# Kernel optimization log

Hardware: AMD Instinct MI355X
Metric: run time of the kernel (lower is better)

## Reference

```python
import jax, jax.numpy as jnp
import numpy as np

N, C, H, W = 512, 512, 7, 7
K = 64
ALPHA = 100.0
HW = H * W


def _up13(x):
    # bilinear upsample (..., 7, 7) -> (..., 13, 13), align_corners=True
    src = jnp.arange(13, dtype=jnp.float32) * (6.0 / 12.0)
    i0 = jnp.floor(src).astype(jnp.int32)
    i1 = jnp.minimum(i0 + 1, 6)
    w = src - i0.astype(jnp.float32)
    xr = x[..., i0, :] * (1.0 - w)[:, None] + x[..., i1, :] * w[:, None]  # rows
    xc = xr[..., :, i0] * (1.0 - w) + xr[..., :, i1] * w                  # cols
    return xc


def _conv2d(x, w, b, p):
    y = jax.lax.conv_general_dilated(
        x, w, window_strides=(1, 1), padding=[(p, p), (p, p)],
        dimension_numbers=('NCHW', 'OIHW', 'NCHW'))
    return y + b[None, :, None, None]


def setup_inputs() -> dict:
    key = jax.random.key(0)
    ks = jax.random.split(key, 16)
    x = jax.random.normal(ks[0], (N, C, H, W), jnp.float32)
    centroids = jax.random.uniform(ks[1], (K, C), jnp.float32)
    # conv params initialized from centroids as in _init_params (separate params after init)
    conv_w = 2.0 * ALPHA * centroids                    # (K, C) 1x1 conv kernel
    conv_b = -ALPHA * jnp.linalg.norm(centroids, axis=1)
    ln_w = jnp.ones((7, 7), jnp.float32)
    ln_b = jnp.zeros((7, 7), jnp.float32)
    c3_w = 0.02 * jax.random.normal(ks[2], (32, 512, 3, 3), jnp.float32)
    c3_b = jnp.zeros((32,), jnp.float32)
    c5_w = 0.02 * jax.random.normal(ks[3], (32, 512, 5, 5), jnp.float32)
    c5_b = jnp.zeros((32,), jnp.float32)
    c7_w = 0.02 * jax.random.normal(ks[4], (20, 512, 7, 7), jnp.float32)
    c7_b = jnp.zeros((20,), jnp.float32)
    dw_w = 0.1 * jax.random.normal(ks[5], (7, 13), jnp.float32)
    dw_b = jnp.zeros((7,), jnp.float32)
    dh_w = 0.1 * jax.random.normal(ks[6], (7, 13), jnp.float32)
    dh_b = jnp.zeros((7,), jnp.float32)
    acc_w = 0.1 * jax.random.normal(ks[7], (1, 84), jnp.float32)  # 1x1 conv (O, I)
    acc_b = jnp.zeros((1,), jnp.float32)
    return dict(x=x, centroids=centroids, conv_w=conv_w, conv_b=conv_b,
                ln_w=ln_w, ln_b=ln_b, c3_w=c3_w, c3_b=c3_b, c5_w=c5_w, c5_b=c5_b,
                c7_w=c7_w, c7_b=c7_b, dw_w=dw_w, dw_b=dw_b, dh_w=dh_w, dh_b=dh_b,
                acc_w=acc_w, acc_b=acc_b)


def reference(x, centroids, conv_w, conv_b, ln_w, ln_b,
              c3_w, c3_b, c5_w, c5_b, c7_w, c7_b,
              dw_w, dw_b, dh_w, dh_b, acc_w, acc_b):
    # ---- CRN on the raw (un-normalized) input ----
    mu = jnp.mean(x, axis=(-2, -1), keepdims=True)
    var = jnp.mean((x - mu) ** 2, axis=(-2, -1), keepdims=True)
    h = (x - mu) / jnp.sqrt(var + 1e-5) * ln_w + ln_b          # LayerNorm([7,7])
    h = _up13(h)                                               # (N,512,13,13)
    h = jnp.concatenate([_conv2d(h, c3_w, c3_b, 1),
                         _conv2d(h, c5_w, c5_b, 2),
                         _conv2d(h, c7_w, c7_b, 3)], axis=1)   # (N,84,13,13)
    h = jnp.einsum('nchw,ow->ncho', h, dw_w) + dw_b            # width 13->7
    h = h.transpose(0, 1, 3, 2)
    h = jnp.einsum('nchw,ow->ncho', h, dh_w) + dh_b            # height 13->7
    cw = jnp.einsum('nchw,oc->nohw', h, acc_w) + acc_b[None, :, None, None]
    cw = cw.reshape(N, 1, HW)                                  # context weights

    # ---- descriptor-wise L2 normalization over channels ----
    nrm = jnp.sqrt(jnp.sum(x * x, axis=1, keepdims=True))
    xn = x / jnp.maximum(nrm, 1e-12)

    # ---- soft assignment (1x1 conv + softmax over clusters) ----
    logits = (jnp.einsum('nchw,kc->nkhw', xn, conv_w)
              + conv_b[None, :, None, None]).reshape(N, K, HW)
    sa = jax.nn.softmax(logits, axis=1)
    mask = sa * cw                                             # (N,K,HW)

    # ---- fused VLAD aggregation (same math as masked residual sum) ----
    xf = xn.reshape(N, C, HW)
    vlad = jnp.einsum('nkl,ncl->nkc', mask, xf) \
        - centroids[None, :, :] * jnp.sum(mask, axis=-1)[:, :, None]
    vlad = vlad / jnp.maximum(jnp.linalg.norm(vlad, axis=2, keepdims=True), 1e-12)
    vlad = vlad.reshape(N, K * C)
    vlad = vlad / jnp.maximum(jnp.linalg.norm(vlad, axis=1, keepdims=True), 1e-12)
    return vlad
```

## Files before the change

kernel.cpp:

```cpp
#include <hip/hip_runtime.h>
#include <math.h>

#define NI 512
#define CC 512
#define KCL 64
#define HW49 49
#define CQ 25088
#define XHP 260
#define AP 260
#define GP 68
#define NKS 256

__device__ __forceinline__ float Uval(int i, int u) {
    if (i & 1) return (u == ((i - 1) >> 1) || u == ((i + 1) >> 1)) ? 0.5f : 0.0f;
    return (u == (i >> 1)) ? 1.0f : 0.0f;
}

__global__ __launch_bounds__(256) void kG(
    const float* __restrict__ c3w, const float* __restrict__ c5w, const float* __restrict__ c7w,
    const float* __restrict__ dww, const float* __restrict__ dhw, const float* __restrict__ accw,
    const float* __restrict__ lnw, const float* __restrict__ lnb,
    float* __restrict__ Gmat, float* __restrict__ Gl)
{
    const int c = blockIdx.x;
    const int t = threadIdx.x;
    __shared__ float dh[91], dw[91];
    __shared__ float Fh3[147], Fw3[147], Fh5[245], Fw5[245], Fh7[343], Fw7[343];
    __shared__ float wa3[9], wa5[25], wa7[49];
    __shared__ float Gtmp[2401];
    if (t < 91) dh[t] = dhw[t];
    if (t >= 128 && t < 219) dw[t - 128] = dww[t - 128];
    __syncthreads();
    for (int idx = t; idx < 147; idx += 256) {
        int oh = idx / 21, r = idx % 21, u = r / 3, dy = r % 3;
        float sh = 0.f, sw = 0.f;
        for (int i = 0; i < 13; i++) { int y = i - dy + 1; if (y >= 0 && y < 13) { float uu = Uval(i, u); sh += dh[oh * 13 + y] * uu; sw += dw[oh * 13 + y] * uu; } }
        Fh3[idx] = sh; Fw3[idx] = sw;
    }
    for (int idx = t; idx < 245; idx += 256) {
        int oh = idx / 35, r = idx % 35, u = r / 5, dy = r % 5;
        float sh = 0.f, sw = 0.f;
        for (int i = 0; i < 13; i++) { int y = i - dy + 2; if (y >= 0 && y < 13) { float uu = Uval(i, u); sh += dh[oh * 13 + y] * uu; sw += dw[oh * 13 + y] * uu; } }
        Fh5[idx] = sh; Fw5[idx] = sw;
    }
    for (int idx = t; idx < 343; idx += 256) {
        int oh = idx / 49, r = idx % 49, u = r / 7, dy = r % 7;
        float sh = 0.f, sw = 0.f;
        for (int i = 0; i < 13; i++) { int y = i - dy + 3; if (y >= 0 && y < 13) { float uu = Uval(i, u); sh += dh[oh * 13 + y] * uu; sw += dw[oh * 13 + y] * uu; } }
        Fh7[idx] = sh; Fw7[idx] = sw;
    }
    if (t < 9)               { float s = 0.f; for (int co = 0; co < 32; co++) s += accw[co]      * c3w[(size_t)(co * 512 + c) * 9  + t];        wa3[t] = s; }
    if (t >= 32 && t < 57)   { int q = t - 32; float s = 0.f; for (int co = 0; co < 32; co++) s += accw[32 + co] * c5w[(size_t)(co * 512 + c) * 25 + q]; wa5[q] = s; }
    if (t >= 64 && t < 113)  { int q = t - 64; float s = 0.f; for (int co = 0; co < 20; co++) s += accw[64 + co] * c7w[(size_t)(co * 512 + c) * 49 + q]; wa7[q] = s; }
    __syncthreads();
    for (int o = t; o < 2401; o += 256) {
        int q = o / 49, p = o % 49;
        int u = q / 7, v = q % 7, ow = p / 7, oh = p % 7;
        float acc = 0.f;
        #pragma unroll
        for (int dy = 0; dy < 3; dy++) { float fh = Fh3[(oh * 7 + u) * 3 + dy];
            #pragma unroll
            for (int dx = 0; dx < 3; dx++) acc += wa3[dy * 3 + dx] * fh * Fw3[(ow * 7 + v) * 3 + dx]; }
        #pragma unroll
        for (int dy = 0; dy < 5; dy++) { float fh = Fh5[(oh * 7 + u) * 5 + dy];
            #pragma unroll
            for (int dx = 0; dx < 5; dx++) acc += wa5[dy * 5 + dx] * fh * Fw5[(ow * 7 + v) * 5 + dx]; }
        #pragma unroll
        for (int dy = 0; dy < 7; dy++) { float fh = Fh7[(oh * 7 + u) * 7 + dy];
            #pragma unroll
            for (int dx = 0; dx < 7; dx++) acc += wa7[dy * 7 + dx] * fh * Fw7[(ow * 7 + v) * 7 + dx]; }
        Gtmp[o] = acc;
        Gmat[(size_t)c * 2401 + o] = acc * lnw[q];
    }
    __syncthreads();
    if (t < 49) {
        float s = 0.f;
        for (int q = 0; q < 49; q++) s += Gtmp[q * 49 + t] * lnb[q];
        Gl[c * 49 + t] = s;
    }
}

__global__ void kCb(const float* __restrict__ c3b, const float* __restrict__ c5b, const float* __restrict__ c7b,
                    const float* __restrict__ dww, const float* __restrict__ dwb,
                    const float* __restrict__ dhw, const float* __restrict__ dhb,
                    const float* __restrict__ accw, const float* __restrict__ accb,
                    const float* __restrict__ Gl, float* __restrict__ Cb)
{
    __shared__ float A0s, A1s, Sdw[7], Sdh[7];
    int t = threadIdx.x;
    if (t == 0) {
        float a0 = 0.f, a1 = 0.f;
        for (int co = 0; co < 84; co++) {
            float aw = accw[co]; a0 += aw;
            float b = (co < 32) ? c3b[co] : ((co < 64) ? c5b[co - 32] : c7b[co - 64]);
            a1 += aw * b;
        }
        A0s = a0; A1s = a1;
    }
    if (t < 7)             { float s = 0.f; for (int xx = 0; xx < 13; xx++) s += dww[t * 13 + xx]; Sdw[t] = s; }
    if (t >= 8 && t < 15)  { int oh = t - 8; float s = 0.f; for (int y = 0; y < 13; y++) s += dhw[oh * 13 + y]; Sdh[oh] = s; }
    __syncthreads();
    if (t < 49) {
        int ow = t / 7, oh = t % 7;
        float g = 0.f;
        for (int c = 0; c < 512; c++) g += Gl[c * 49 + t];
        Cb[t] = A1s * Sdw[ow] * Sdh[oh] + A0s * (dwb[ow] * Sdh[oh] + dhb[oh]) + accb[0] + g;
    }
}

__global__ __launch_bounds__(256) void kCw1(const float* __restrict__ x,
    const float* __restrict__ Gmat, float* __restrict__ part)
{
    __shared__ float As[49 * AP];
    __shared__ float Gs[49 * GP];
    const int b = blockIdx.x;
    const int nt = b >> 8, ks = b & 255;
    const int n0 = nt * 256;
    const int t = threadIdx.x;
    const int tn = t >> 3;
    const int tp = t & 7;
    float acc[8][8];
    #pragma unroll
    for (int j = 0; j < 8; j++)
        #pragma unroll
        for (int m = 0; m < 8; m++) acc[j][m] = 0.f;
    for (int kk = 0; kk < 2; kk++) {
        const int c = ks * 2 + kk;
        for (int i = t; i < 12544; i += 256) {
            int nr = i / 49, q = i - nr * 49;
            As[q * AP + nr] = x[(size_t)(n0 + nr) * CQ + (size_t)c * 49 + q];
        }
        for (int i = t; i < 2401; i += 256) {
            int q = i / 49, p = i - q * 49;
            Gs[q * GP + p] = Gmat[(size_t)c * 2401 + i];
        }
        for (int i = t; i < 735; i += 256) {
            int q = i / 15, pc = 49 + (i - q * 15);
            Gs[q * GP + pc] = 0.f;
        }
        __syncthreads();
        {
            float s = 0.f, ss = 0.f;
            for (int q = 0; q < 49; q++) { float v = As[q * AP + t]; s += v; ss += v * v; }
            float mu = s * (1.f / 49.f);
            float var = ss * (1.f / 49.f) - mu * mu;
            float rs = 1.f / sqrtf(var + 1e-5f);
            for (int q = 0; q < 49; q++) As[q * AP + t] = (As[q * AP + t] - mu) * rs;
        }
        __syncthreads();
        for (int q = 0; q < 49; q++) {
            float4 a0 = *(const float4*)&As[q * AP + tn * 8];
            float4 a1 = *(const float4*)&As[q * AP + tn * 8 + 4];
            float4 g0 = *(const float4*)&Gs[q * GP + tp * 8];
            float4 g1 = *(const float4*)&Gs[q * GP + tp * 8 + 4];
            float av[8] = {a0.x, a0.y, a0.z, a0.w, a1.x, a1.y, a1.z, a1.w};
            float gv[8] = {g0.x, g0.y, g0.z, g0.w, g1.x, g1.y, g1.z, g1.w};
            #pragma unroll
            for (int j = 0; j < 8; j++)
                #pragma unroll
                for (int m = 0; m < 8; m++) acc[j][m] += av[j] * gv[m];
        }
        __syncthreads();
    }
    #pragma unroll
    for (int j = 0; j < 8; j++) {
        #pragma unroll
        for (int m = 0; m < 8; m++) {
            int p = tp * 8 + m;
            if (p < 49) As[(tn * 8 + j) * 49 + p] = acc[j][m];
        }
    }
    __syncthreads();
    {
        float* dst = part + (size_t)ks * CQ + (size_t)n0 * 49;
        for (int i = t; i < 12544; i += 256) dst[i] = As[i];
    }
}

__global__ __launch_bounds__(512, 2) void kMain(const float* __restrict__ x,
    const float* __restrict__ convw, const float* __restrict__ convb,
    const float* __restrict__ part, const float* __restrict__ Cbg,
    const float* __restrict__ cent, float* __restrict__ out)
{
    __shared__ float xH[49 * XHP];
    __shared__ float lg[64 * 52];
    __shared__ float ps[8 * 56];
    __shared__ float rn[49], cwl[49], smax[49], sinv[49];
    __shared__ float cb[64];
    __shared__ float pmx[392], psm[392];
    __shared__ float msL[64], ssq[64], scl[64];
    const int n = blockIdx.x;
    const int t = threadIdx.x;
    const int lane = t & 63;
    const int w = t >> 6;
    const float* xp = x + (size_t)n * CQ;

    if (t < 392) {
        int p = t >> 3, q = t & 7;
        const float* bp = part + (size_t)n * 49 + p;
        float s = 0.f;
        for (int ks = q * 32; ks < q * 32 + 32; ks++) s += bp[(size_t)ks * CQ];
        psm[t] = s;
    }
    if (t >= 448) cb[t - 448] = convb[t - 448];
    __syncthreads();
    if (t < 49) {
        float s = Cbg[t];
        #pragma unroll
        for (int q = 0; q < 8; q++) s += psm[t * 8 + q];
        cwl[t] = s;
    }

    float a[8];
    #pragma unroll
    for (int j = 0; j < 8; j++) a[j] = 0.f;
    float rs_part = 0.f;
    const int kw = __builtin_amdgcn_readfirstlane(w);

    for (int half = 0; half < 2; half++) {
        const int cbase = half * 256;
        __syncthreads();
        for (int idx = t; idx < 3136; idx += 512) {
            int l = idx % 49, cg = idx / 49;
            const float* src = xp + (size_t)(cbase + cg * 4) * 49 + l;
            float4 v;
            v.x = src[0]; v.y = src[49]; v.z = src[98]; v.w = src[147];
            *(float4*)&xH[l * XHP + cg * 4] = v;
        }
        __syncthreads();
        if (lane < 49) {
            const float* row = &xH[lane * XHP + kw * 32];
            float s = 0.f;
            #pragma unroll
            for (int c4 = 0; c4 < 8; c4++) {
                float4 v = *(const float4*)(row + c4 * 4);
                s += v.x * v.x + v.y * v.y + v.z * v.z + v.w * v.w;
            }
            rs_part += s;
        }
        {
            const int lr = (lane < 49) ? lane : 48;
            const float* xrow = &xH[lr * XHP];
            const float* wb = convw + (size_t)(kw * 8) * 512 + cbase;
            #pragma unroll 4
            for (int c4 = 0; c4 < 64; c4++) {
                float4 xv = *(const float4*)(xrow + c4 * 4);
                #pragma unroll
                for (int j = 0; j < 8; j++) {
                    float4 wv = *(const float4*)&wb[(size_t)j * 512 + c4 * 4];
                    a[j] += wv.x * xv.x + wv.y * xv.y + wv.z * xv.z + wv.w * xv.w;
                }
            }
        }
    }
    if (lane < 49) ps[kw * 56 + lane] = rs_part;
    __syncthreads();
    if (t < 49) {
        float s = 0.f;
        #pragma unroll
        for (int q = 0; q < 8; q++) s += ps[q * 56 + t];
        rn[t] = 1.f / fmaxf(sqrtf(s), 1e-12f);
    }
    __syncthreads();
    if (lane < 49) {
        float r = rn[lane];
        #pragma unroll
        for (int j = 0; j < 8; j++) lg[(kw * 8 + j) * 52 + lane] = a[j] * r + cb[kw * 8 + j];
    }
    __syncthreads();
    if (t < 392) {
        int l = t >> 3, kq = t & 7;
        float m = -3.402823466e38f;
        #pragma unroll
        for (int j = 0; j < 8; j++) m = fmaxf(m, lg[(kq * 8 + j) * 52 + l]);
        pmx[t] = m;
    }
    __syncthreads();
    if (t < 49) {
        float m = pmx[t * 8];
        #pragma unroll
        for (int q = 1; q < 8; q++) m = fmaxf(m, pmx[t * 8 + q]);
        smax[t] = m;
    }
    __syncthreads();
    if (t < 392) {
        int l = t >> 3, kq = t & 7;
        float m = smax[l], s = 0.f;
        #pragma unroll
        for (int j = 0; j < 8; j++) s += __expf(lg[(kq * 8 + j) * 52 + l] - m);
        psm[t] = s;
    }
    __syncthreads();
    if (t < 49) {
        float s = 0.f;
        #pragma unroll
        for (int q = 0; q < 8; q++) s += psm[t * 8 + q];
        sinv[t] = 1.f / s;
    }
    __syncthreads();
    if (t < 392) {
        int l = t >> 3, kq = t & 7;
        float m = smax[l], si = sinv[l] * cwl[l];
        #pragma unroll
        for (int j = 0; j < 8; j++) {
            int idx = (kq * 8 + j) * 52 + l;
            lg[idx] = __expf(lg[idx] - m) * si;
        }
    }
    __syncthreads();
    if (t < 64) {
        float s = 0.f;
        for (int l = 0; l < 49; l++) s += lg[t * 52 + l];
        msL[t] = s;
    }
    __syncthreads();
    if (t < 392) {
        int l = t >> 3, kq = t & 7;
        float r = rn[l];
        #pragma unroll
        for (int j = 0; j < 8; j++) lg[(kq * 8 + j) * 52 + l] *= r;
    }
    __syncthreads();
    const int c0 = lane * 4;
    float accB[8][4], accA[8][4];
    #pragma unroll
    for (int j = 0; j < 8; j++)
        #pragma unroll
        for (int ci = 0; ci < 4; ci++) { accB[j][ci] = 0.f; accA[j][ci] = 0.f; }
    #pragma unroll 7
    for (int l = 0; l < 49; l++) {
        float4 xv = *(const float4*)&xH[l * XHP + c0];
        #pragma unroll
        for (int j = 0; j < 8; j++) {
            float m = lg[(kw * 8 + j) * 52 + l];
            accB[j][0] += m * xv.x; accB[j][1] += m * xv.y; accB[j][2] += m * xv.z; accB[j][3] += m * xv.w;
        }
    }
    __syncthreads();
    for (int idx = t; idx < 3136; idx += 512) {
        int l = idx % 49, cg = idx / 49;
        const float* src = xp + (size_t)(cg * 4) * 49 + l;
        float4 v;
        v.x = src[0]; v.y = src[49]; v.z = src[98]; v.w = src[147];
        *(float4*)&xH[l * XHP + cg * 4] = v;
    }
    __syncthreads();
    #pragma unroll 7
    for (int l = 0; l < 49; l++) {
        float4 xv = *(const float4*)&xH[l * XHP + c0];
        #pragma unroll
        for (int j = 0; j < 8; j++) {
            float m = lg[(kw * 8 + j) * 52 + l];
            accA[j][0] += m * xv.x; accA[j][1] += m * xv.y; accA[j][2] += m * xv.z; accA[j][3] += m * xv.w;
        }
    }
    float ssr[8];
    #pragma unroll
    for (int j = 0; j < 8; j++) {
        int k = kw * 8 + j;
        float ms = msL[k];
        float4 ca = *(const float4*)&cent[(size_t)k * 512 + c0];
        float4 cbv = *(const float4*)&cent[(size_t)k * 512 + 256 + c0];
        accA[j][0] -= ca.x * ms; accA[j][1] -= ca.y * ms; accA[j][2] -= ca.z * ms; accA[j][3] -= ca.w * ms;
        accB[j][0] -= cbv.x * ms; accB[j][1] -= cbv.y * ms; accB[j][2] -= cbv.z * ms; accB[j][3] -= cbv.w * ms;
        float s = 0.f;
        #pragma unroll
        for (int ci = 0; ci < 4; ci++) s += accA[j][ci] * accA[j][ci] + accB[j][ci] * accB[j][ci];
        ssr[j] = s;
    }
    #pragma unroll
    for (int j = 0; j < 8; j++)
        for (int off = 32; off >= 1; off >>= 1) ssr[j] += __shfl_xor(ssr[j], off, 64);
    if (lane == 0) {
        #pragma unroll
        for (int j = 0; j < 8; j++) ssq[kw * 8 + j] = ssr[j];
    }
    __syncthreads();
    if (t < 64) {
        float nrm = sqrtf(ssq[t]);
        float inv = 1.f / fmaxf(nrm, 1e-12f);
        float sk = nrm * inv;
        float g = sk * sk;
        #pragma unroll
        for (int off = 32; off >= 1; off >>= 1) g += __shfl_xor(g, off, 64);
        scl[t] = inv * (1.f / fmaxf(sqrtf(g), 1e-12f));
    }
    __syncthreads();
    #pragma unroll
    for (int j = 0; j < 8; j++) {
        int k = kw * 8 + j;
        float s2 = scl[k];
        float4 o1 = make_float4(accA[j][0] * s2, accA[j][1] * s2, accA[j][2] * s2, accA[j][3] * s2);
        float4 o2 = make_float4(accB[j][0] * s2, accB[j][1] * s2, accB[j][2] * s2, accB[j][3] * s2);
        *(float4*)&out[(size_t)n * 32768 + (size_t)k * 512 + c0] = o1;
        *(float4*)&out[(size_t)n * 32768 + (size_t)k * 512 + 256 + c0] = o2;
    }
}

extern "C" void kernel_launch(void* const* d_in, const int* in_sizes, int n_in,
                              void* d_out, int out_size, void* d_ws, size_t ws_size,
                              hipStream_t stream)
{
    const float* x     = (const float*)d_in[0];
    const float* cent  = (const float*)d_in[1];
    const float* convw = (const float*)d_in[2];
    const float* convb = (const float*)d_in[3];
    const float* lnw   = (const float*)d_in[4];
    const float* lnb   = (const float*)d_in[5];
    const float* c3w   = (const float*)d_in[6];
    const float* c3b   = (const float*)d_in[7];
    const float* c5w   = (const float*)d_in[8];
    const float* c5b   = (const float*)d_in[9];
    const float* c7w   = (const float*)d_in[10];
    const float* c7b   = (const float*)d_in[11];
    const float* dww   = (const float*)d_in[12];
    const float* dwb   = (const float*)d_in[13];
    const float* dhw   = (const float*)d_in[14];
    const float* dhb   = (const float*)d_in[15];
    const float* accw  = (const float*)d_in[16];
    const float* accb  = (const float*)d_in[17];
    float* out = (float*)d_out;

    char* ws = (char*)d_ws;
    float* Gmat = (float*)(ws);
    float* Gl   = (float*)(ws + 4917248);
    float* Cb   = (float*)(ws + 5017600);
    float* part = (float*)(ws + 5017856);

    kG   <<<512, 256, 0, stream>>>(c3w, c5w, c7w, dww, dhw, accw, lnw, lnb, Gmat, Gl);
    kCb  <<<1,   64,  0, stream>>>(c3b, c5b, c7b, dww, dwb, dhw, dhb, accw, accb, Gl, Cb);
    kCw1 <<<512, 256, 0, stream>>>(x, Gmat, part);
    kMain<<<512, 512, 0, stream>>>(x, convw, convb, part, Cb, cent, out);
}
```

Before: 220.8 us.

## Stage conv weights in LDS per channel quarter and fold norm scaling into x reload

```diff
diff --git a/kernel.cpp b/kernel.cpp
--- a/kernel.cpp
+++ b/kernel.cpp
@@ -6,10 +6,11 @@
 #define KCL 64
 #define HW49 49
 #define CQ 25088
-#define XHP 260
 #define AP 260
 #define GP 68
-#define NKS 256
+#define XQP 132
+#define WOFF 6468
+#define XHP 260
 
 __device__ __forceinline__ float Uval(int i, int u) {
     if (i & 1) return (u == ((i - 1) >> 1) || u == ((i + 1) >> 1)) ? 0.5f : 0.0f;
@@ -182,25 +183,31 @@
     const float* __restrict__ part, const float* __restrict__ Cbg,
     const float* __restrict__ cent, float* __restrict__ out)
 {
-    __shared__ float xH[49 * XHP];
+    __shared__ float big[14660];
     __shared__ float lg[64 * 52];
     __shared__ float ps[8 * 56];
     __shared__ float rn[49], cwl[49], smax[49], sinv[49];
     __shared__ float cb[64];
     __shared__ float pmx[392], psm[392];
-    __shared__ float msL[64], ssq[64], scl[64];
+    __shared__ float ssq[64], scl[64];
     const int n = blockIdx.x;
     const int t = threadIdx.x;
     const int lane = t & 63;
     const int w = t >> 6;
+    const int kw = __builtin_amdgcn_readfirstlane(w);
     const float* xp = x + (size_t)n * CQ;
 
     if (t < 392) {
         int p = t >> 3, q = t & 7;
-        const float* bp = part + (size_t)n * 49 + p;
-        float s = 0.f;
-        for (int ks = q * 32; ks < q * 32 + 32; ks++) s += bp[(size_t)ks * CQ];
-        psm[t] = s;
+        const float* bp = part + (size_t)(q * 32) * CQ + (size_t)n * 49 + p;
+        float s0 = 0.f, s1 = 0.f, s2 = 0.f, s3 = 0.f;
+        for (int i = 0; i < 32; i += 4) {
+            s0 += bp[(size_t)(i + 0) * CQ];
+            s1 += bp[(size_t)(i + 1) * CQ];
+            s2 += bp[(size_t)(i + 2) * CQ];
+            s3 += bp[(size_t)(i + 3) * CQ];
+        }
+        psm[t] = (s0 + s1) + (s2 + s3);
     }
     if (t >= 448) cb[t - 448] = convb[t - 448];
     __syncthreads();
@@ -215,39 +222,41 @@
     #pragma unroll
     for (int j = 0; j < 8; j++) a[j] = 0.f;
     float rs_part = 0.f;
-    const int kw = __builtin_amdgcn_readfirstlane(w);
-
-    for (int half = 0; half < 2; half++) {
-        const int cbase = half * 256;
+
+    for (int qt = 0; qt < 4; qt++) {
+        const int qb = qt * 128;
         __syncthreads();
-        for (int idx = t; idx < 3136; idx += 512) {
-            int l = idx % 49, cg = idx / 49;
-            const float* src = xp + (size_t)(cbase + cg * 4) * 49 + l;
+        for (int idx = t; idx < 1568; idx += 512) {
+            int cg = idx / 49, l = idx - cg * 49;
+            const float* src = xp + (size_t)(qb + cg * 4) * 49 + l;
             float4 v;
             v.x = src[0]; v.y = src[49]; v.z = src[98]; v.w = src[147];
-            *(float4*)&xH[l * XHP + cg * 4] = v;
+            *(float4*)&big[l * XQP + cg * 4] = v;
+        }
+        for (int idx = t; idx < 2048; idx += 512) {
+            int k = idx >> 5, c4 = idx & 31;
+            *(float4*)&big[WOFF + k * 128 + c4 * 4] =
+                *(const float4*)&convw[(size_t)k * 512 + qb + c4 * 4];
         }
         __syncthreads();
         if (lane < 49) {
-            const float* row = &xH[lane * XHP + kw * 32];
-            float s = 0.f;
+            const float* row = &big[lane * XQP + kw * 16];
             #pragma unroll
-            for (int c4 = 0; c4 < 8; c4++) {
+            for (int c4 = 0; c4 < 4; c4++) {
                 float4 v = *(const float4*)(row + c4 * 4);
-                s += v.x * v.x + v.y * v.y + v.z * v.z + v.w * v.w;
+                rs_part += v.x * v.x + v.y * v.y + v.z * v.z + v.w * v.w;
             }
-            rs_part += s;
         }
         {
             const int lr = (lane < 49) ? lane : 48;
-            const float* xrow = &xH[lr * XHP];
-            const float* wb = convw + (size_t)(kw * 8) * 512 + cbase;
+            const float* xrow = &big[lr * XQP];
+            const float* wrow = &big[WOFF + kw * 1024];
             #pragma unroll 4
-            for (int c4 = 0; c4 < 64; c4++) {
+            for (int c4 = 0; c4 < 32; c4++) {
                 float4 xv = *(const float4*)(xrow + c4 * 4);
                 #pragma unroll
                 for (int j = 0; j < 8; j++) {
-                    float4 wv = *(const float4*)&wb[(size_t)j * 512 + c4 * 4];
+                    float4 wv = *(const float4*)&wrow[j * 128 + c4 * 4];
                     a[j] += wv.x * xv.x + wv.y * xv.y + wv.z * xv.z + wv.w * xv.w;
                 }
             }
@@ -308,28 +317,31 @@
         }
     }
     __syncthreads();
-    if (t < 64) {
+    float msr[8];
+    #pragma unroll
+    for (int j = 0; j < 8; j++) {
         float s = 0.f;
-        for (int l = 0; l < 49; l++) s += lg[t * 52 + l];
-        msL[t] = s;
-    }
-    __syncthreads();
-    if (t < 392) {
-        int l = t >> 3, kq = t & 7;
+        for (int l = 0; l < 49; l++) s += lg[(kw * 8 + j) * 52 + l];
+        msr[j] = s;
+    }
+    const int c0 = lane * 4;
+    float accA[8][4], accB[8][4];
+    #pragma unroll
+    for (int j = 0; j < 8; j++)
+        #pragma unroll
+        for (int ci = 0; ci < 4; ci++) { accA[j][ci] = 0.f; accB[j][ci] = 0.f; }
+    for (int idx = t; idx < 3136; idx += 512) {
+        int cg = idx / 49, l = idx - cg * 49;
+        const float* src = xp + (size_t)(256 + cg * 4) * 49 + l;
+        float4 v;
         float r = rn[l];
-        #pragma unroll
-        for (int j = 0; j < 8; j++) lg[(kq * 8 + j) * 52 + l] *= r;
-    }
-    __syncthreads();
-    const int c0 = lane * 4;
-    float accB[8][4], accA[8][4];
-    #pragma unroll
-    for (int j = 0; j < 8; j++)
-        #pragma unroll
-        for (int ci = 0; ci < 4; ci++) { accB[j][ci] = 0.f; accA[j][ci] = 0.f; }
+        v.x = src[0] * r; v.y = src[49] * r; v.z = src[98] * r; v.w = src[147] * r;
+        *(float4*)&big[l * XHP + cg * 4] = v;
+    }
+    __syncthreads();
     #pragma unroll 7
     for (int l = 0; l < 49; l++) {
-        float4 xv = *(const float4*)&xH[l * XHP + c0];
+        float4 xv = *(const float4*)&big[l * XHP + c0];
         #pragma unroll
         for (int j = 0; j < 8; j++) {
             float m = lg[(kw * 8 + j) * 52 + l];
@@ -338,16 +350,17 @@
     }
     __syncthreads();
     for (int idx = t; idx < 3136; idx += 512) {
-        int l = idx % 49, cg = idx / 49;
+        int cg = idx / 49, l = idx - cg * 49;
         const float* src = xp + (size_t)(cg * 4) * 49 + l;
         float4 v;
-        v.x = src[0]; v.y = src[49]; v.z = src[98]; v.w = src[147];
-        *(float4*)&xH[l * XHP + cg * 4] = v;
+        float r = rn[l];
+        v.x = src[0] * r; v.y = src[49] * r; v.z = src[98] * r; v.w = src[147] * r;
+        *(float4*)&big[l * XHP + cg * 4] = v;
     }
     __syncthreads();
     #pragma unroll 7
     for (int l = 0; l < 49; l++) {
-        float4 xv = *(const float4*)&xH[l * XHP + c0];
+        float4 xv = *(const float4*)&big[l * XHP + c0];
         #pragma unroll
         for (int j = 0; j < 8; j++) {
             float m = lg[(kw * 8 + j) * 52 + l];
@@ -358,7 +371,7 @@
     #pragma unroll
     for (int j = 0; j < 8; j++) {
         int k = kw * 8 + j;
-        float ms = msL[k];
+        float ms = msr[j];
         float4 ca = *(const float4*)&cent[(size_t)k * 512 + c0];
         float4 cbv = *(const float4*)&cent[(size_t)k * 512 + 256 + c0];
         accA[j][0] -= ca.x * ms; accA[j][1] -= ca.y * ms; accA[j][2] -= ca.z * ms; accA[j][3] -= ca.w * ms;
```

Result: slower. 300.5 us (+36.1%).
